# Performance work log

Hardware: AMD Instinct MI355X
Metric: run time of the kernel (lower is better)

## Reference

```python
import jax, jax.numpy as jnp
import numpy as np

N_NODES = 100000
N_EDGES = 1600000
IN_DIM = 128
OUT_DIM = 128
ALPHA = 0.2  # leaky relu negative slope
EPS = 9e-15


def setup_inputs() -> dict:
    key = jax.random.key(0)
    k1, k2, k3, k4, k5 = jax.random.split(key, 5)
    x = jax.random.normal(k1, (N_NODES, IN_DIM), dtype=jnp.float32)
    src = jax.random.randint(k2, (N_EDGES,), 0, N_NODES)
    dst = jax.random.randint(k3, (N_EDGES,), 0, N_NODES)
    edge_index = jnp.stack([src, dst]).astype(jnp.int64)
    # xavier-normal-ish params
    W = jax.random.normal(k4, (IN_DIM, OUT_DIM), dtype=jnp.float32) * (1.414 * np.sqrt(2.0 / (IN_DIM + OUT_DIM)))
    attn = jax.random.normal(k5, (1, 2 * OUT_DIM), dtype=jnp.float32) * (1.414 * np.sqrt(2.0 / (1 + 2 * OUT_DIM)))
    return {"x": x, "edge_index": edge_index, "W": W, "attn": attn}


def reference(x, edge_index, W, attn):
    N = x.shape[0]
    h = x @ W  # [N, out_dim]
    d = h.shape[1]
    a_src, a_dst = attn[0, :d], attn[0, d:]
    src, dst = edge_index[0], edge_index[1]
    # attn @ cat(h[src], h[dst]) == (h @ a_src)[src] + (h @ a_dst)[dst]
    values = (h @ a_src)[src] + (h @ a_dst)[dst]  # [E]
    e_a = jnp.where(values > 0, values, ALPHA * values)  # leaky relu
    edge_e = jnp.exp(e_a - jnp.max(e_a))  # [E]
    rowsum = jax.ops.segment_sum(edge_e, src, num_segments=N)  # [N]
    h_prime = jax.ops.segment_sum(edge_e[:, None] * h[dst], src, num_segments=N)  # [N, d]
    h_prime = h_prime / (rowsum[:, None] + EPS)
    return jax.nn.elu(h_prime)
```

## Files before the change

### kernel.cpp

```cpp
#include <hip/hip_runtime.h>
#include <hip/hip_bf16.h>
#include <stdint.h>


#define NN 100000
#define NE 1600000
#define DIM 128
#define ALPHA_ 0.2f
#define EPS_ 9e-15f

#define NB 1563
#define CHUNK 2048
#define NPART 782
#define NGEMM 1564
#define SDEG 56

typedef short bf16x8 __attribute__((ext_vector_type(8)));
typedef float floatx4 __attribute__((ext_vector_type(4)));

static __device__ __forceinline__ float bflo(unsigned u){ return __uint_as_float(u << 16); }
static __device__ __forceinline__ float bfhi(unsigned u){ return __uint_as_float(u & 0xFFFF0000u); }
static __device__ __forceinline__ float bfs(unsigned short s){ return __uint_as_float((unsigned)s << 16); }
static __device__ __forceinline__ unsigned short f2bf(float f){
  unsigned b = __float_as_uint(f);
  unsigned r = (b + 0x7FFFu + ((b >> 16) & 1u)) >> 16;
  return (unsigned short)r;
}
static __device__ __forceinline__ unsigned short f2bf_rhu(float f){
  return (unsigned short)((__float_as_uint(f) + 0x8000u) >> 16);
}
static __device__ __forceinline__ unsigned fkey(float f){
  unsigned u = __float_as_uint(f);
  return (u & 0x80000000u) ? ~u : (u | 0x80000000u);
}
static __device__ __forceinline__ float dkey(unsigned k){
  unsigned u = (k & 0x80000000u) ? (k ^ 0x80000000u) : ~k;
  return __uint_as_float(u);
}

__global__ __launch_bounds__(256) void k_init(const unsigned short* W, const unsigned* EI,
                                              const unsigned short* attn, int* flags,
                                              unsigned short* attnb, unsigned short* Wt){
  __shared__ int sh_f, sh_e;
  int b = blockIdx.x, tid = threadIdx.x;
  if (b == 0){
    if (tid == 0){ sh_f = 0; sh_e = 0; }
    __syncthreads();
    for (int i = tid; i < 1024; i += 256){
      unsigned u = W[i];
      if (((u >> 7) & 0xFF) >= 0x85) sh_f = 1;
    }
    int any = 0;
    for (int k = tid; k < 2048; k += 256) any |= EI[2 * k + 1];
    atomicOr(&sh_e, any);
    __syncthreads();
    if (tid == 0){ flags[0] = sh_f; flags[1] = (sh_e == 0) ? 1 : 0; }
    __syncthreads();
    attnb[tid] = sh_f ? f2bf(((const float*)attn)[tid]) : attn[tid];
  } else {
    if (tid == 0) sh_f = 0;
    __syncthreads();
    for (int i = tid; i < 1024; i += 256){
      unsigned u = W[i];
      if (((u >> 7) & 0xFF) >= 0x85) sh_f = 1;
    }
    __syncthreads();
    int i = (b - 1) * 256 + tid;
    int k = i >> 7, n = i & 127;
    unsigned short v = sh_f ? f2bf(((const float*)W)[i]) : ((const unsigned short*)W)[i];
    Wt[n * DIM + k] = v;
  }
}

static __device__ __forceinline__ void load_edge(const int* EI, int e64, int e,
                                                 int& s, int& d){
  if (e64){
    const long long* E64 = (const long long*)EI;
    s = (int)E64[e];
    d = (int)E64[NE + e];
  } else {
    s = EI[e];
    d = EI[NE + e];
  }
}

static __device__ __forceinline__ void gemm_path(int gid, char* smem,
                                                 const void* X, const int* flags,
                                                 const unsigned short* Wt,
                                                 const unsigned short* attnb,
                                                 unsigned short* H, float* s1, float* s2,
                                                 float* gmax1, float* gmax2){
  char* wlds = smem;
  float* sm1 = (float*)(smem + 16384);
  float* sm2 = sm1 + 4;
  int tid = threadIdx.x;
  int wid = tid >> 6, lane = tid & 63;
  int m = lane & 15, q = lane >> 4;
  int rb = gid * 64 + wid * 16;
  int row = rb + m;
  bool rok = row < NN;
  int fx32 = flags[0];

  floatx4 acc[8];
  #pragma unroll
  for (int t = 0; t < 8; t++){ acc[t][0]=0.f; acc[t][1]=0.f; acc[t][2]=0.f; acc[t][3]=0.f; }

  for (int hk = 0; hk < 2; hk++){
    float4 f0, f1, f2, f3;
    bf16x8 a0, a1;
    if (rok){
      if (fx32){
        const float* xr = (const float*)X + (size_t)row * DIM + hk * 64 + q * 8;
        f0 = ((const float4*)xr)[0];
        f1 = ((const float4*)xr)[1];
        f2 = ((const float4*)(xr + 32))[0];
        f3 = ((const float4*)(xr + 32))[1];
      } else {
        const unsigned short* xr = (const unsigned short*)X + (size_t)row * DIM + hk * 64 + q * 8;
        a0 = *(const bf16x8*)xr;
        a1 = *(const bf16x8*)(xr + 32);
      }
    }
    for (int j = tid; j < 1024; j += 256){
      int wr = j >> 3, c = j & 7;
      uint4 v = ((const uint4*)Wt)[wr * 16 + hk * 8 + c];
      *(uint4*)(wlds + ((wr * 8 + (c ^ (wr & 7))) << 4)) = v;
    }
    __syncthreads();
    bf16x8 fr[2];
    #pragma unroll
    for (int j = 0; j < 8; j++){ fr[0][j] = 0; fr[1][j] = 0; }
    if (rok){
      if (fx32){
        fr[0][0] = (short)f2bf_rhu(f0.x); fr[0][1] = (short)f2bf_rhu(f0.y);
        fr[0][2] = (short)f2bf_rhu(f0.z); fr[0][3] = (short)f2bf_rhu(f0.w);
        fr[0][4] = (short)f2bf_rhu(f1.x); fr[0][5] = (short)f2bf_rhu(f1.y);
        fr[0][6] = (short)f2bf_rhu(f1.z); fr[0][7] = (short)f2bf_rhu(f1.w);
        fr[1][0] = (short)f2bf_rhu(f2.x); fr[1][1] = (short)f2bf_rhu(f2.y);
        fr[1][2] = (short)f2bf_rhu(f2.z); fr[1][3] = (short)f2bf_rhu(f2.w);
        fr[1][4] = (short)f2bf_rhu(f3.x); fr[1][5] = (short)f2bf_rhu(f3.y);
        fr[1][6] = (short)f2bf_rhu(f3.z); fr[1][7] = (short)f2bf_rhu(f3.w);
      } else {
        fr[0] = a0; fr[1] = a1;
      }
    }
    #pragma unroll
    for (int ki2 = 0; ki2 < 2; ki2++){
      #pragma unroll
      for (int t = 0; t < 8; t++){
        int rowb = t * 16 + m;
        bf16x8 bfr = *(const bf16x8*)(wlds + ((rowb * 8 + ((ki2 * 4 + q) ^ (m & 7))) << 4));
        acc[t] = __builtin_amdgcn_mfma_f32_16x16x32_bf16(fr[ki2], bfr, acc[t], 0, 0, 0);
      }
    }
    __syncthreads();
  }

  float as[8], ad[8];
  #pragma unroll
  for (int t = 0; t < 8; t++){
    as[t] = bfs(attnb[t * 16 + m]);
    ad[t] = bfs(attnb[DIM + t * 16 + m]);
  }
  float lm1 = -3.0e38f, lm2 = -3.0e38f;
  #pragma unroll
  for (int r = 0; r < 4; r++){
    int grow = rb + q * 4 + r;
    float p1 = 0.f, p2 = 0.f;
    #pragma unroll
    for (int t = 0; t < 8; t++){ p1 += acc[t][r] * as[t]; p2 += acc[t][r] * ad[t]; }
    #pragma unroll
    for (int off = 1; off < 16; off <<= 1){
      p1 += __shfl_xor(p1, off);
      p2 += __shfl_xor(p2, off);
    }
    if (grow < NN){
      if (m == 0){ s1[grow] = p1; s2[grow] = p2; }
      lm1 = fmaxf(lm1, p1); lm2 = fmaxf(lm2, p2);
    }
  }
  #pragma unroll
  for (int off = 32; off; off >>= 1){
    lm1 = fmaxf(lm1, __shfl_xor(lm1, off));
    lm2 = fmaxf(lm2, __shfl_xor(lm2, off));
  }
  if (lane == 0){ sm1[wid] = lm1; sm2[wid] = lm2; }
  __syncthreads();
  if (tid == 0){
    gmax1[gid] = fmaxf(fmaxf(sm1[0], sm1[1]), fmaxf(sm1[2], sm1[3]));
    gmax2[gid] = fmaxf(fmaxf(sm2[0], sm2[1]), fmaxf(sm2[2], sm2[3]));
  }

  char* wb = wlds + wid * 4096;
  #pragma unroll
  for (int r = 0; r < 4; r++){
    int trow = q * 4 + r;
    #pragma unroll
    for (int t = 0; t < 8; t++){
      int col = t * 16 + m;
      int boff = trow * 256 + (((((col >> 3) ^ trow) & 15)) << 4) + ((col & 7) << 1);
      *(unsigned short*)(wb + boff) = f2bf(acc[t][r]);
    }
  }
  __syncthreads();
  int lrow = lane >> 2;
  int grow2 = rb + lrow;
  #pragma unroll
  for (int u = 0; u < 4; u++){
    int c = u * 4 + (lane & 3);
    uint4 v = *(const uint4*)(wb + lrow * 256 + (((c ^ lrow) & 15) << 4));
    if (grow2 < NN) *(uint4*)(H + (size_t)grow2 * DIM + c * 8) = v;
  }
}

static __device__ __forceinline__ void part_path(int pid, char* smem,
                                                 const int* EI, const int* flags,
                                                 unsigned* dir, unsigned* sout_g){
  unsigned* sout = (unsigned*)smem;
  int* hist = (int*)(smem + 8192);
  int tid = threadIdx.x;
  int e0 = pid * CHUNK;
  int nmy = NE - e0; if (nmy > CHUNK) nmy = CHUNK;
  int e64 = flags[1];

  for (int i = tid; i < NB; i += 256) hist[i] = 0;
  __syncthreads();

  unsigned ent[8]; int bv[8];
  #pragma unroll
  for (int i = 0; i < 8; i++){
    int idx = tid + i * 256;
    if (idx < nmy){
      int s, d;
      load_edge(EI, e64, e0 + idx, s, d);
      ent[i] = ((unsigned)(s & 63) << 17) | (unsigned)d;
      bv[i] = s >> 6;
      atomicAdd(&hist[bv[i]], 1);
    } else {
      ent[i] = 0u; bv[i] = -1;
    }
  }
  __syncthreads();

  if (tid < 64){
    int carry = 0;
    for (int rr = 0; rr < (NB + 63) / 64; rr++){
      int idx = rr * 64 + tid;
      int v = (idx < NB) ? hist[idx] : 0;
      int x = v;
      #pragma unroll
      for (int off = 1; off < 64; off <<= 1){
        int y = __shfl_up(x, off);
        if (tid >= off) x += y;
      }
      if (idx < NB) hist[idx] = x - v + carry;
      carry += __shfl(x, 63);
    }
    if (tid == 0) hist[NB] = carry;
  }
  __syncthreads();

  for (int t = tid; t < NB; t += 256){
    unsigned ls = (unsigned)hist[t];
    unsigned len = (unsigned)(hist[t + 1] - hist[t]);
    dir[(size_t)pid * NB + t] = (ls << 16) | len;
  }
  __syncthreads();

  #pragma unroll
  for (int i = 0; i < 8; i++){
    if (bv[i] >= 0){
      int p = atomicAdd(&hist[bv[i]], 1);
      sout[p] = ent[i];
    }
  }
  __syncthreads();

  for (int i = tid * 4; i < nmy; i += 1024)
    *(uint4*)(sout_g + e0 + i) = *(const uint4*)(sout + i);
}

__global__ __launch_bounds__(256, 6) void k_main(const void* X, const int* EI,
                                                 const int* flags,
                                                 const unsigned short* Wt,
                                                 const unsigned short* attnb,
                                                 unsigned short* H, float* s1, float* s2,
                                                 float* gmax1, float* gmax2,
                                                 unsigned* dir, unsigned* sout_g){
  __shared__ char smem[16448];
  int bid = blockIdx.x;
  int T = bid / 3, r = bid % 3;
  if (r == 2){
    part_path(T, smem, EI, flags, dir, sout_g);
  } else {
    gemm_path(T * 2 + r, smem, X, flags, Wt, attnb, H, s1, s2, gmax1, gmax2);
  }
}

__global__ __launch_bounds__(256) void k_maxs(const float* gmax1, const float* gmax2,
                                              unsigned* keys){
  int tid = threadIdx.x;
  float a = -3.0e38f, b = -3.0e38f;
  for (int i = tid; i < NGEMM; i += 256){
    a = fmaxf(a, gmax1[i]);
    b = fmaxf(b, gmax2[i]);
  }
  #pragma unroll
  for (int off = 32; off; off >>= 1){
    a = fmaxf(a, __shfl_xor(a, off));
    b = fmaxf(b, __shfl_xor(b, off));
  }
  __shared__ float m1[4], m2[4];
  int lane = tid & 63, wid = tid >> 6;
  if (lane == 0){ m1[wid] = a; m2[wid] = b; }
  __syncthreads();
  if (tid == 0){
    keys[0] = fkey(fmaxf(fmaxf(m1[0], m1[1]), fmaxf(m1[2], m1[3])));
    keys[1] = fkey(fmaxf(fmaxf(m2[0], m2[1]), fmaxf(m2[2], m2[3])));
  }
}

__global__ __launch_bounds__(256) void k_sbagg(const unsigned* dir, const unsigned* sout_g,
                                               const float* s1, const float* s2,
                                               const unsigned* keys,
                                               const unsigned short* H, float* out){
  __shared__ int lcnt[64];
  __shared__ int llist[64][SDEG];
  int B = blockIdx.x;
  int tid = threadIdx.x;
  if (tid < 64) lcnt[tid] = 0;
  __syncthreads();
  for (int b = tid; b < NPART; b += 256){
    unsigned dv = dir[(size_t)b * NB + B];
    int len = (int)(dv & 0xFFFFu);
    if (len){
      const unsigned* sp = sout_g + (size_t)b * CHUNK + (dv >> 16);
      for (int j = 0; j < len; j++){
        unsigned ent = sp[j];
        int sl = ent >> 17;
        int p = atomicAdd(&lcnt[sl], 1);
        if (p < SDEG) llist[sl][p] = ent & 0x1FFFF;
      }
    }
  }
  __syncthreads();
  float V = dkey(keys[0]) + dkey(keys[1]);
  float M = V > 0.f ? V : ALPHA_ * V;
  int wid = tid >> 6, lane = tid & 63;
  const unsigned* h2 = (const unsigned*)H;
  for (int sl = wid; sl < 64; sl += 4){
    int srcn = B * 64 + sl;
    if (srcn >= NN) break;
    int deg = lcnt[sl]; if (deg > SDEG) deg = SDEG;
    float s1n = s1[srcn];
    int pd = 0; float pw = 0.f;
    if (lane < deg){
      pd = llist[sl][lane];
      float v = s1n + s2[pd];
      float va = v > 0.f ? v : ALPHA_ * v;
      pw = __expf(va - M);
    }
    float a0 = 0.f, a1 = 0.f, wsum = 0.f;
    int j = 0;
    for (; j + 4 <= deg; j += 4){
      int d0 = __shfl(pd, j), d1 = __shfl(pd, j + 1), d2 = __shfl(pd, j + 2), d3 = __shfl(pd, j + 3);
      float w0 = __shfl(pw, j), w1 = __shfl(pw, j + 1), w2 = __shfl(pw, j + 2), w3 = __shfl(pw, j + 3);
      unsigned v0 = h2[d0 * 64 + lane];
      unsigned v1 = h2[d1 * 64 + lane];
      unsigned v2 = h2[d2 * 64 + lane];
      unsigned v3 = h2[d3 * 64 + lane];
      a0 += w0 * bflo(v0) + w1 * bflo(v1) + w2 * bflo(v2) + w3 * bflo(v3);
      a1 += w0 * bfhi(v0) + w1 * bfhi(v1) + w2 * bfhi(v2) + w3 * bfhi(v3);
      wsum += (w0 + w1) + (w2 + w3);
    }
    for (; j < deg; j++){
      int d = __shfl(pd, j); float w = __shfl(pw, j);
      unsigned v = h2[d * 64 + lane];
      a0 += w * bflo(v); a1 += w * bfhi(v); wsum += w;
    }
    float r = wsum + EPS_;
    float p0 = a0 / r, p1 = a1 / r;
    float o0 = p0 > 0.f ? p0 : expm1f(p0);
    float o1 = p1 > 0.f ? p1 : expm1f(p1);
    ((float2*)out)[srcn * 64 + lane] = make_float2(o0, o1);
  }
}

extern "C" void kernel_launch(void* const* d_in, const int* in_sizes, int n_in,
                              void* d_out, int out_size, void* d_ws, size_t ws_size,
                              hipStream_t stream){
  (void)in_sizes; (void)n_in; (void)out_size; (void)ws_size;
  const void* X    = d_in[0];
  const int*  EI   = (const int*)d_in[1];
  const void* W    = d_in[2];
  const void* attn = d_in[3];

  char* ws = (char*)d_ws;
  size_t off = 0;
  auto alloc = [&](size_t bytes) -> char* {
    char* p = ws + off;
    off += (bytes + 255) & ~(size_t)255;
    return p;
  };
  unsigned short* H      = (unsigned short*)alloc((size_t)NN * DIM * 2);
  unsigned*       sout_g = (unsigned*)alloc((size_t)NE * 4);
  unsigned*       dir    = (unsigned*)alloc((size_t)NPART * NB * 4);
  unsigned short* Wt     = (unsigned short*)alloc(DIM * DIM * 2);
  unsigned short* attnb  = (unsigned short*)alloc(256 * 2);
  int*            flags  = (int*)alloc(2 * 4);
  float*          s1     = (float*)alloc(NN * 4);
  float*          s2     = (float*)alloc(NN * 4);
  float*          gmax1  = (float*)alloc(NGEMM * 4);
  float*          gmax2  = (float*)alloc(NGEMM * 4);
  unsigned*       keys   = (unsigned*)alloc(2 * 4);
  float*          outp   = (float*)d_out;

  k_init<<<65, 256, 0, stream>>>((const unsigned short*)W, (const unsigned*)EI,
                                 (const unsigned short*)attn, flags, attnb, Wt);
  k_main<<<NPART * 3, 256, 0, stream>>>(X, EI, flags, Wt, attnb, H, s1, s2,
                                        gmax1, gmax2, dir, sout_g);
  k_maxs<<<1, 256, 0, stream>>>(gmax1, gmax2, keys);
  k_sbagg<<<NB, 256, 0, stream>>>(dir, sout_g, s1, s2, keys, H, outp);
}
```

Before: 219.7 us.

## Double partition chunk size and transpose the bucket directory for coalesced reads

Partition blocks now bin 4096 edges each instead of 2048, which halves the number of partitions and the size of the directory. k_main's block mix changes to four GEMM blocks per partition block. The max-reduction kernel is merged with a new tiled transpose of the directory, so k_sbagg reads each bucket's entries contiguously instead of with stride NB. This adds one transpose pass and more shared memory per k_main block, which may lower occupancy.

```diff
diff --git a/kernel.cpp b/kernel.cpp
--- a/kernel.cpp
+++ b/kernel.cpp
@@ -10,8 +10,8 @@
 #define EPS_ 9e-15f
 
 #define NB 1563
-#define CHUNK 2048
-#define NPART 782
+#define CHUNK 4096
+#define NPART 391
 #define NGEMM 1564
 #define SDEG 56
 
@@ -217,7 +217,7 @@
                                                  const int* EI, const int* flags,
                                                  unsigned* dir, unsigned* sout_g){
   unsigned* sout = (unsigned*)smem;
-  int* hist = (int*)(smem + 8192);
+  int* hist = (int*)(smem + 16384);
   int tid = threadIdx.x;
   int e0 = pid * CHUNK;
   int nmy = NE - e0; if (nmy > CHUNK) nmy = CHUNK;
@@ -226,9 +226,9 @@
   for (int i = tid; i < NB; i += 256) hist[i] = 0;
   __syncthreads();
 
-  unsigned ent[8]; int bv[8];
-  #pragma unroll
-  for (int i = 0; i < 8; i++){
+  unsigned ent[16]; int bv[16];
+  #pragma unroll
+  for (int i = 0; i < 16; i++){
     int idx = tid + i * 256;
     if (idx < nmy){
       int s, d;
@@ -268,7 +268,7 @@
   __syncthreads();
 
   #pragma unroll
-  for (int i = 0; i < 8; i++){
+  for (int i = 0; i < 16; i++){
     if (bv[i] >= 0){
       int p = atomicAdd(&hist[bv[i]], 1);
       sout[p] = ent[i];
@@ -287,40 +287,62 @@
                                                  unsigned short* H, float* s1, float* s2,
                                                  float* gmax1, float* gmax2,
                                                  unsigned* dir, unsigned* sout_g){
-  __shared__ char smem[16448];
+  __shared__ char smem[22656];
   int bid = blockIdx.x;
-  int T = bid / 3, r = bid % 3;
-  if (r == 2){
+  int T = bid / 5, r = bid % 5;
+  if (r == 4){
     part_path(T, smem, EI, flags, dir, sout_g);
   } else {
-    gemm_path(T * 2 + r, smem, X, flags, Wt, attnb, H, s1, s2, gmax1, gmax2);
-  }
-}
-
-__global__ __launch_bounds__(256) void k_maxs(const float* gmax1, const float* gmax2,
-                                              unsigned* keys){
-  int tid = threadIdx.x;
-  float a = -3.0e38f, b = -3.0e38f;
-  for (int i = tid; i < NGEMM; i += 256){
-    a = fmaxf(a, gmax1[i]);
-    b = fmaxf(b, gmax2[i]);
-  }
-  #pragma unroll
-  for (int off = 32; off; off >>= 1){
-    a = fmaxf(a, __shfl_xor(a, off));
-    b = fmaxf(b, __shfl_xor(b, off));
-  }
-  __shared__ float m1[4], m2[4];
-  int lane = tid & 63, wid = tid >> 6;
-  if (lane == 0){ m1[wid] = a; m2[wid] = b; }
-  __syncthreads();
-  if (tid == 0){
-    keys[0] = fkey(fmaxf(fmaxf(m1[0], m1[1]), fmaxf(m1[2], m1[3])));
-    keys[1] = fkey(fmaxf(fmaxf(m2[0], m2[1]), fmaxf(m2[2], m2[3])));
-  }
-}
-
-__global__ __launch_bounds__(256) void k_sbagg(const unsigned* dir, const unsigned* sout_g,
+    gemm_path(T * 4 + r, smem, X, flags, Wt, attnb, H, s1, s2, gmax1, gmax2);
+  }
+}
+
+__global__ __launch_bounds__(256) void k_aux(const float* gmax1, const float* gmax2,
+                                             unsigned* keys, const unsigned* dir,
+                                             unsigned* dir_t){
+  int b = blockIdx.x, tid = threadIdx.x;
+  if (b == 0){
+    float a = -3.0e38f, bb = -3.0e38f;
+    for (int i = tid; i < NGEMM; i += 256){
+      a = fmaxf(a, gmax1[i]);
+      bb = fmaxf(bb, gmax2[i]);
+    }
+    #pragma unroll
+    for (int off = 32; off; off >>= 1){
+      a = fmaxf(a, __shfl_xor(a, off));
+      bb = fmaxf(bb, __shfl_xor(bb, off));
+    }
+    __shared__ float m1[4], m2[4];
+    int lane = tid & 63, wid = tid >> 6;
+    if (lane == 0){ m1[wid] = a; m2[wid] = bb; }
+    __syncthreads();
+    if (tid == 0){
+      keys[0] = fkey(fmaxf(fmaxf(m1[0], m1[1]), fmaxf(m1[2], m1[3])));
+      keys[1] = fkey(fmaxf(fmaxf(m2[0], m2[1]), fmaxf(m2[2], m2[3])));
+    }
+  } else {
+    __shared__ unsigned tile[64][65];
+    int tb = b - 1;
+    int tc = tb % 25;
+    int tr = tb / 25;
+    int r0 = tr * 64, c0 = tc * 64;
+    int cc = tid & 63;
+    for (int rr = tid >> 6; rr < 64; rr += 4){
+      int gp = r0 + rr, gB = c0 + cc;
+      unsigned v = 0;
+      if (gp < NPART && gB < NB) v = dir[(size_t)gp * NB + gB];
+      tile[rr][cc] = v;
+    }
+    __syncthreads();
+    for (int rr = tid >> 6; rr < 64; rr += 4){
+      int gB = c0 + rr, gp = r0 + cc;
+      if (gB < NB && gp < NPART)
+        dir_t[(size_t)gB * NPART + gp] = tile[cc][rr];
+    }
+  }
+}
+
+__global__ __launch_bounds__(256) void k_sbagg(const unsigned* dir_t, const unsigned* sout_g,
                                                const float* s1, const float* s2,
                                                const unsigned* keys,
                                                const unsigned short* H, float* out){
@@ -330,16 +352,16 @@
   int tid = threadIdx.x;
   if (tid < 64) lcnt[tid] = 0;
   __syncthreads();
-  for (int b = tid; b < NPART; b += 256){
-    unsigned dv = dir[(size_t)b * NB + B];
+  for (int p = tid; p < NPART; p += 256){
+    unsigned dv = dir_t[(size_t)B * NPART + p];
     int len = (int)(dv & 0xFFFFu);
     if (len){
-      const unsigned* sp = sout_g + (size_t)b * CHUNK + (dv >> 16);
+      const unsigned* sp = sout_g + (size_t)p * CHUNK + (dv >> 16);
       for (int j = 0; j < len; j++){
         unsigned ent = sp[j];
         int sl = ent >> 17;
-        int p = atomicAdd(&lcnt[sl], 1);
-        if (p < SDEG) llist[sl][p] = ent & 0x1FFFF;
+        int pos = atomicAdd(&lcnt[sl], 1);
+        if (pos < SDEG) llist[sl][pos] = ent & 0x1FFFF;
       }
     }
   }
@@ -405,6 +427,7 @@
   unsigned short* H      = (unsigned short*)alloc((size_t)NN * DIM * 2);
   unsigned*       sout_g = (unsigned*)alloc((size_t)NE * 4);
   unsigned*       dir    = (unsigned*)alloc((size_t)NPART * NB * 4);
+  unsigned*       dir_t  = (unsigned*)alloc((size_t)NB * NPART * 4);
   unsigned short* Wt     = (unsigned short*)alloc(DIM * DIM * 2);
   unsigned short* attnb  = (unsigned short*)alloc(256 * 2);
   int*            flags  = (int*)alloc(2 * 4);
@@ -417,8 +440,8 @@
 
   k_init<<<65, 256, 0, stream>>>((const unsigned short*)W, (const unsigned*)EI,
                                  (const unsigned short*)attn, flags, attnb, Wt);
-  k_main<<<NPART * 3, 256, 0, stream>>>(X, EI, flags, Wt, attnb, H, s1, s2,
+  k_main<<<NPART * 5, 256, 0, stream>>>(X, EI, flags, Wt, attnb, H, s1, s2,
                                         gmax1, gmax2, dir, sout_g);
-  k_maxs<<<1, 256, 0, stream>>>(gmax1, gmax2, keys);
-  k_sbagg<<<NB, 256, 0, stream>>>(dir, sout_g, s1, s2, keys, H, outp);
-}
+  k_aux<<<1 + 7 * 25, 256, 0, stream>>>(gmax1, gmax2, keys, dir, dir_t);
+  k_sbagg<<<NB, 256, 0, stream>>>(dir_t, sout_g, s1, s2, keys, H, outp);
+}
```

Measured after the change: 219.4 us. About the same (-0.1%).
